# Kernel tuning notes

Hardware: AMD Instinct MI355X
Metric: run time of the kernel (lower is better)

Reference implementation:

```python
import jax, jax.numpy as jnp
import numpy as np

R = 8192            # reservoir_size
CORE = int(R * 0.6)          # 4915
SHELL = int(R * 0.3)         # 2457
FB = R - CORE - SHELL        # 820
H = 1024            # lstm_hidden
IN = 1              # input_size
OUT = 1             # output_size
LEAK = 0.1
SPECTRAL = 0.9
SPARSITY = 0.3


def _scaled(key, n):
    # uniform(-1,1) NxN; spectral radius of such a matrix ~ sqrt(n * var) = sqrt(n/3).
    # Scale to ~SPECTRAL (mimics the SVD-based scaling at init without the O(n^3) SVD).
    W = jax.random.uniform(key, (n, n), jnp.float32, -1.0, 1.0)
    return W * (SPECTRAL / jnp.sqrt(n / 3.0))


def setup_inputs() -> dict:
    key = jax.random.key(0)
    ks = jax.random.split(key, 20)
    u = lambda k, sh: jax.random.uniform(k, sh, jnp.float32, -1.0, 1.0)

    W_in = u(ks[0], (R, IN))
    W_core = _scaled(ks[1], CORE)
    mask_shell = (jax.random.uniform(ks[2], (SHELL, SHELL)) < SPARSITY).astype(jnp.float32)
    W_shell = _scaled(ks[3], SHELL) * mask_shell
    W_feedback = _scaled(ks[4], FB)
    W_shell_core = u(ks[5], (CORE, SHELL))
    W_feedback_core = u(ks[6], (CORE, FB))
    dopamine = jnp.float32(0.5)
    omega = jnp.ones((R,), jnp.float32) * 2.0
    gamma = jnp.ones((R,), jnp.float32) * 0.1

    # PyTorch LSTM params, gate order [i, f, g, o]
    s = 1.0 / np.sqrt(H)
    W_ih = jax.random.uniform(ks[7], (4 * H, R), jnp.float32, -s, s)
    W_hh = jax.random.uniform(ks[8], (4 * H, H), jnp.float32, -s, s)
    b_ih = jax.random.uniform(ks[9], (4 * H,), jnp.float32, -s, s)
    b_hh = jax.random.uniform(ks[10], (4 * H,), jnp.float32, -s, s)

    W_out = jax.random.uniform(ks[11], (OUT, H), jnp.float32, -s, s)
    b_out = jax.random.uniform(ks[12], (OUT,), jnp.float32, -s, s)

    x = jax.random.normal(ks[13], (IN,), jnp.float32)
    state = jax.random.normal(ks[14], (1, R), jnp.float32)
    lstm_hidden = jax.random.normal(ks[15], (1, 1, H), jnp.float32)
    lstm_cell = jax.random.normal(ks[16], (1, 1, H), jnp.float32)

    return dict(x=x, state=state, lstm_hidden=lstm_hidden, lstm_cell=lstm_cell,
                W_in=W_in, W_core=W_core, W_shell=W_shell, W_feedback=W_feedback,
                W_shell_core=W_shell_core, W_feedback_core=W_feedback_core,
                dopamine=dopamine, omega=omega, gamma=gamma,
                W_ih=W_ih, W_hh=W_hh, b_ih=b_ih, b_hh=b_hh,
                W_out=W_out, b_out=b_out)


def reference(x, state, lstm_hidden, lstm_cell,
              W_in, W_core, W_shell, W_feedback, W_shell_core, W_feedback_core,
              dopamine, omega, gamma, W_ih, W_hh, b_ih, b_hh, W_out, b_out):
    reservoir_in = W_in @ x                      # (R,)
    core = state[:, :CORE]                       # (1, CORE)
    shell = state[:, CORE:CORE + SHELL]          # (1, SHELL)
    fb = state[:, -FB:]                          # (1, FB)

    core_pred = jnp.tanh(core @ W_core.T + reservoir_in[:CORE][None, :])
    shell_pred = jnp.tanh(shell @ W_shell.T)
    fb_pred = jnp.tanh(fb @ W_feedback.T)
    core_pred = core_pred + jnp.tanh(shell_pred @ W_shell_core.T) \
                          + jnp.tanh(fb_pred @ W_feedback_core.T)

    core_new = (1.0 - LEAK) * core + LEAK * core_pred
    shell_new = (1.0 - LEAK) * shell + LEAK * shell_pred
    fb_new = (1.0 - LEAK) * fb + LEAK * fb_pred
    s = jnp.concatenate([core_new, shell_new, fb_new], axis=1)  # (1, R)

    # harmonic oscillator update + dopamine scaling
    s = s + 0.1 * (omega * s - gamma * jnp.tanh(s))
    s = dopamine * s

    # single LSTM cell step (torch gate order i, f, g, o)
    h = lstm_hidden[0]  # (1, H)
    c = lstm_cell[0]    # (1, H)
    gates = s @ W_ih.T + b_ih + h @ W_hh.T + b_hh   # (1, 4H)
    i, f, g, o = jnp.split(gates, 4, axis=1)
    c_new = jax.nn.sigmoid(f) * c + jax.nn.sigmoid(i) * jnp.tanh(g)
    h_new = jax.nn.sigmoid(o) * jnp.tanh(c_new)

    output = h_new @ W_out.T + b_out             # (1, OUT)
    return output, s, h_new[None], c_new[None]
```

## Files before the change

kernel.cpp:

```cpp
#include <hip/hip_runtime.h>
#include <math.h>

#define R_TOT 8192
#define CORE  4915
#define SHELL 2457
#define FB    820
#define H     1024

__device__ float g_pred1[R_TOT];
__device__ float g_s[R_TOT];
__device__ float g_gates[4 * H];

__device__ __forceinline__ int swz(int i) { return i + (i >> 5); }
#define SWZ_SIZE(n) ((n) + (((n) - 1) >> 5))

__device__ __forceinline__ float waveReduce(float v) {
  #pragma unroll
  for (int off = 32; off; off >>= 1) v += __shfl_down(v, off, 64);
  return v;
}

__device__ __forceinline__ float dotRow(const float* __restrict__ w,
                                        const float* __restrict__ xs,
                                        int xb, int N, int lane) {
  uintptr_t a = (uintptr_t)w;
  int head = (int)(((16 - (a & 15)) & 15) >> 2);
  if (head > N) head = N;
  float s0 = 0.f, s1 = 0.f, s2 = 0.f, s3 = 0.f;
  if (lane < head) s0 += w[lane] * xs[swz(xb + lane)];
  int nC = (N - head) >> 2;
  const float4* wv = (const float4*)(w + head);
  int b0 = xb + head;
  int c = lane;
  for (; c + 192 < nC; c += 256) {
    float4 v0 = wv[c], v1 = wv[c + 64], v2 = wv[c + 128], v3 = wv[c + 192];
    int i0 = b0 + (c << 2);
    s0 += v0.x*xs[swz(i0    )] + v0.y*xs[swz(i0+  1)] + v0.z*xs[swz(i0+  2)] + v0.w*xs[swz(i0+  3)];
    s1 += v1.x*xs[swz(i0+256)] + v1.y*xs[swz(i0+257)] + v1.z*xs[swz(i0+258)] + v1.w*xs[swz(i0+259)];
    s2 += v2.x*xs[swz(i0+512)] + v2.y*xs[swz(i0+513)] + v2.z*xs[swz(i0+514)] + v2.w*xs[swz(i0+515)];
    s3 += v3.x*xs[swz(i0+768)] + v3.y*xs[swz(i0+769)] + v3.z*xs[swz(i0+770)] + v3.w*xs[swz(i0+771)];
  }
  for (; c < nC; c += 64) {
    float4 v = wv[c];
    int i0 = b0 + (c << 2);
    s1 += v.x*xs[swz(i0)] + v.y*xs[swz(i0+1)] + v.z*xs[swz(i0+2)] + v.w*xs[swz(i0+3)];
  }
  for (int i = head + (nC << 2) + lane; i < N; i += 64)
    s2 += w[i] * xs[swz(xb + i)];
  return (s0 + s1) + (s2 + s3);
}

#define NB1_CORE  ((CORE  + 3) / 4)
#define NB1_SHELL ((SHELL + 3) / 4)
#define NB1_FB    ((FB    + 3) / 4)

__global__ __launch_bounds__(256, 8) void k_stage1(
    const float* __restrict__ state, const float* __restrict__ Wcore,
    const float* __restrict__ Wshell, const float* __restrict__ Wfb,
    const float* __restrict__ Win, const float* __restrict__ xin) {
  __shared__ float xs[SWZ_SIZE(CORE)];
  int b = blockIdx.x;
  int rowBase, N, xoff, isCore = 0;
  const float* W;
  if (b < NB1_CORE)                  { rowBase = b * 4;                         N = CORE;  xoff = 0;            W = Wcore; isCore = 1; }
  else if (b < NB1_CORE + NB1_SHELL) { rowBase = (b - NB1_CORE) * 4;            N = SHELL; xoff = CORE;         W = Wshell; }
  else                               { rowBase = (b - NB1_CORE - NB1_SHELL)*4;  N = FB;    xoff = CORE + SHELL; W = Wfb; }
  for (int i = threadIdx.x; i < N; i += 256) xs[swz(i)] = state[xoff + i];
  __syncthreads();
  int wave = threadIdx.x >> 6, lane = threadIdx.x & 63;
  int r = rowBase + wave;
  if (r >= N) return;
  float sum = waveReduce(dotRow(W + (size_t)r * N, xs, 0, N, lane));
  if (lane == 0) {
    if (isCore) sum += Win[r] * xin[0];
    g_pred1[xoff + r] = tanhf(sum);
  }
}

#define NB2_CORE ((CORE + 3) / 4)
#define NB2_EW   ((SHELL + FB + 255) / 256)

__device__ __forceinline__ void s_update(int i, float pred,
                                         const float* __restrict__ state,
                                         const float* __restrict__ omega,
                                         const float* __restrict__ gamma,
                                         float dopa, float* __restrict__ dout) {
  float old = state[i];
  float s1 = 0.9f * old + 0.1f * pred;
  float s2 = s1 + 0.1f * (omega[i] * s1 - gamma[i] * tanhf(s1));
  float s3 = dopa * s2;
  g_s[i] = s3;
  dout[1 + i] = s3;
}

__global__ __launch_bounds__(256, 8) void k_stage2(
    const float* __restrict__ state,
    const float* __restrict__ Wsc, const float* __restrict__ Wfc,
    const float* __restrict__ omega, const float* __restrict__ gamma,
    const float* __restrict__ dopamine, float* __restrict__ dout) {
  __shared__ float xs[SWZ_SIZE(SHELL + FB)];
  float dopa = dopamine[0];
  int b = blockIdx.x;
  if (b < NB2_CORE) {
    for (int i = threadIdx.x; i < SHELL + FB; i += 256) xs[swz(i)] = g_pred1[CORE + i];
    __syncthreads();
    int wave = threadIdx.x >> 6, lane = threadIdx.x & 63;
    int r = b * 4 + wave;
    if (r >= CORE) return;
    float d1 = waveReduce(dotRow(Wsc + (size_t)r * SHELL, xs, 0, SHELL, lane));
    float d2 = waveReduce(dotRow(Wfc + (size_t)r * FB, xs, SHELL, FB, lane));
    if (lane == 0) {
      float pred = g_pred1[r] + tanhf(d1) + tanhf(d2);
      s_update(r, pred, state, omega, gamma, dopa, dout);
    }
  } else {
    int i = CORE + (b - NB2_CORE) * 256 + threadIdx.x;
    if (i < R_TOT) s_update(i, g_pred1[i], state, omega, gamma, dopa, dout);
  }
}

__global__ __launch_bounds__(256, 4) void k_gates(
    const float* __restrict__ h,
    const float* __restrict__ Wih, const float* __restrict__ Whh,
    const float* __restrict__ bih, const float* __restrict__ bhh) {
  __shared__ float xs[SWZ_SIZE(R_TOT + H)];
  for (int i = threadIdx.x; i < R_TOT; i += 256) xs[swz(i)] = g_s[i];
  for (int i = threadIdx.x; i < H; i += 256) xs[swz(R_TOT + i)] = h[i];
  __syncthreads();
  int wave = threadIdx.x >> 6, lane = threadIdx.x & 63;
  int r = blockIdx.x * 4 + wave;
  float sum = dotRow(Wih + (size_t)r * R_TOT, xs, 0, R_TOT, lane)
            + dotRow(Whh + (size_t)r * H, xs, R_TOT, H, lane);
  sum = waveReduce(sum);
  if (lane == 0) g_gates[r] = sum + bih[r] + bhh[r];
}

__global__ __launch_bounds__(1024) void k_lstm(
    const float* __restrict__ c_in, const float* __restrict__ Wout,
    const float* __restrict__ bout, float* __restrict__ dout) {
  __shared__ float red[16];
  int j = threadIdx.x;
  float ig = g_gates[j], fg = g_gates[H + j], gg = g_gates[2 * H + j], og = g_gates[3 * H + j];
  float c = c_in[j];
  float cn = (1.f / (1.f + expf(-fg))) * c + (1.f / (1.f + expf(-ig))) * tanhf(gg);
  float hn = (1.f / (1.f + expf(-og))) * tanhf(cn);
  dout[1 + R_TOT + j] = hn;
  dout[1 + R_TOT + H + j] = cn;
  float w = Wout[j] * hn;
  w = waveReduce(w);
  int wave = j >> 6, lane = j & 63;
  if (lane == 0) red[wave] = w;
  __syncthreads();
  if (j == 0) {
    float t = 0.f;
    #pragma unroll
    for (int k = 0; k < 16; ++k) t += red[k];
    dout[0] = t + bout[0];
  }
}

extern "C" void kernel_launch(void* const* d_in, const int* in_sizes, int n_in,
                              void* d_out, int out_size, void* d_ws, size_t ws_size,
                              hipStream_t stream) {
  const float *x = 0, *state = 0, *h = 0, *c = 0, *Win = 0, *Wcore = 0, *Wshell = 0,
              *Wfb = 0, *Wsc = 0, *Wfc = 0, *dopa = 0, *omega = 0, *gamma = 0,
              *Wih = 0, *Whh = 0, *bih = 0, *bhh = 0, *Wout = 0, *bout = 0;
  int n1 = 0, n1024 = 0, n8192 = 0, n4096 = 0;
  for (int i = 0; i < n_in; ++i) {
    const float* p = (const float*)d_in[i];
    switch (in_sizes[i]) {
      case 24157225: Wcore = p; break;
      case 6036849:  Wshell = p; break;
      case 672400:   Wfb = p; break;
      case 12076155: Wsc = p; break;
      case 4030300:  Wfc = p; break;
      case 33554432: Wih = p; break;
      case 4194304:  Whh = p; break;
      case 1:    { if (n1 == 0) x = p; else if (n1 == 1) dopa = p; else bout = p; n1++; } break;
      case 1024: { if (n1024 == 0) h = p; else if (n1024 == 1) c = p; else Wout = p; n1024++; } break;
      case 8192: { if (n8192 == 0) state = p; else if (n8192 == 1) Win = p;
                   else if (n8192 == 2) omega = p; else gamma = p; n8192++; } break;
      case 4096: { if (n4096 == 0) bih = p; else bhh = p; n4096++; } break;
      default: break;
    }
  }
  float* dout = (float*)d_out;

  k_stage1<<<NB1_CORE + NB1_SHELL + NB1_FB, 256, 0, stream>>>(
      state, Wcore, Wshell, Wfb, Win, x);
  k_stage2<<<NB2_CORE + NB2_EW, 256, 0, stream>>>(
      state, Wsc, Wfc, omega, gamma, dopa, dout);
  k_gates<<<(4 * H) / 4, 256, 0, stream>>>(h, Wih, Whh, bih, bhh);
  k_lstm<<<1, 1024, 0, stream>>>(c, Wout, bout, dout);
}
```

Measured before the change: 367.4 us.

## Fuse all stages into one cooperative persistent kernel with atomic work queues

```diff
diff --git a/kernel.cpp b/kernel.cpp
--- a/kernel.cpp
+++ b/kernel.cpp
@@ -1,5 +1,8 @@
 #include <hip/hip_runtime.h>
+#include <hip/hip_cooperative_groups.h>
 #include <math.h>
+
+namespace cg = cooperative_groups;
 
 #define R_TOT 8192
 #define CORE  4915
@@ -7,9 +10,14 @@
 #define FB    820
 #define H     1024
 
-__device__ float g_pred1[R_TOT];
-__device__ float g_s[R_TOT];
-__device__ float g_gates[4 * H];
+#define NBLK  1024
+#define NTHR  256
+
+__device__ __align__(16) float g_pred1[R_TOT];
+__device__ __align__(16) float g_s[R_TOT];
+__device__ __align__(16) float g_gates[4 * H];
+__device__ int g_q1 = 0;
+__device__ int g_q2 = 0;
 
 __device__ __forceinline__ int swz(int i) { return i + (i >> 5); }
 #define SWZ_SIZE(n) ((n) + (((n) - 1) >> 5))
@@ -19,6 +27,8 @@
   for (int off = 32; off; off >>= 1) v += __shfl_down(v, off, 64);
   return v;
 }
+
+__device__ __forceinline__ float sigm(float x) { return 1.f / (1.f + expf(-x)); }
 
 __device__ __forceinline__ float dotRow(const float* __restrict__ w,
                                         const float* __restrict__ xs,
@@ -50,6 +60,146 @@
   return (s0 + s1) + (s2 + s3);
 }
 
+__device__ __forceinline__ void s_update(int i, float pred,
+                                         const float* __restrict__ state,
+                                         const float* __restrict__ omega,
+                                         const float* __restrict__ gamma,
+                                         float dopa, float* __restrict__ dout) {
+  float old = state[i];
+  float s1 = 0.9f * old + 0.1f * pred;
+  float s2 = s1 + 0.1f * (omega[i] * s1 - gamma[i] * tanhf(s1));
+  float s3 = dopa * s2;
+  g_s[i] = s3;
+  dout[1 + i] = s3;
+}
+
+#define P1_SHELL0 CORE
+#define P1_WHH0   (CORE + SHELL)
+#define P1_FB0    (CORE + SHELL + 4 * H)
+#define P1_N      (CORE + SHELL + 4 * H + FB)
+
+__global__ __launch_bounds__(NTHR, 4) void k_fused(
+    const float* __restrict__ state, const float* __restrict__ Wcore,
+    const float* __restrict__ Wshell, const float* __restrict__ Wfb,
+    const float* __restrict__ Win, const float* __restrict__ xin,
+    const float* __restrict__ Wsc, const float* __restrict__ Wfc,
+    const float* __restrict__ omega, const float* __restrict__ gamma,
+    const float* __restrict__ dopamine,
+    const float* __restrict__ Wih, const float* __restrict__ Whh,
+    const float* __restrict__ bih, const float* __restrict__ bhh,
+    const float* __restrict__ hin, const float* __restrict__ cin,
+    const float* __restrict__ Wout, const float* __restrict__ bout,
+    float* __restrict__ dout) {
+  __shared__ float xs[SWZ_SIZE(R_TOT + H)];
+  __shared__ float red[4];
+  cg::grid_group grid = cg::this_grid();
+  const int tid = threadIdx.x, wave = tid >> 6, lane = tid & 63;
+
+  {
+    const float4* s4 = (const float4*)state;
+    for (int i = tid; i < R_TOT / 4; i += NTHR) {
+      float4 v = s4[i]; int b = i << 2;
+      xs[swz(b)] = v.x; xs[swz(b+1)] = v.y; xs[swz(b+2)] = v.z; xs[swz(b+3)] = v.w;
+    }
+    const float4* h4 = (const float4*)hin;
+    for (int i = tid; i < H / 4; i += NTHR) {
+      float4 v = h4[i]; int b = R_TOT + (i << 2);
+      xs[swz(b)] = v.x; xs[swz(b+1)] = v.y; xs[swz(b+2)] = v.z; xs[swz(b+3)] = v.w;
+    }
+  }
+  __syncthreads();
+  const float x0 = xin[0];
+
+  for (;;) {
+    int idx;
+    if (lane == 0) idx = atomicAdd(&g_q1, 1);
+    idx = __shfl(idx, 0, 64);
+    if (idx >= P1_N) break;
+    const float* w; int xb, N; float* dst; float pre = 0.f; int doT = 1;
+    if (idx < P1_SHELL0) {
+      w = Wcore + (size_t)idx * CORE; xb = 0; N = CORE;
+      dst = g_pred1 + idx; pre = Win[idx] * x0;
+    } else if (idx < P1_WHH0) {
+      int r = idx - P1_SHELL0;
+      w = Wshell + (size_t)r * SHELL; xb = CORE; N = SHELL;
+      dst = g_pred1 + CORE + r;
+    } else if (idx < P1_FB0) {
+      int r = idx - P1_WHH0;
+      w = Whh + (size_t)r * H; xb = R_TOT; N = H;
+      dst = g_gates + r; doT = 0;
+    } else {
+      int r = idx - P1_FB0;
+      w = Wfb + (size_t)r * FB; xb = CORE + SHELL; N = FB;
+      dst = g_pred1 + CORE + SHELL + r;
+    }
+    float sum = waveReduce(dotRow(w, xs, xb, N, lane)) + pre;
+    if (lane == 0) *dst = doT ? tanhf(sum) : sum;
+  }
+
+  grid.sync();
+
+  if (blockIdx.x == 0 && tid == 0) atomicExch(&g_q1, 0);
+  const float dopa = dopamine[0];
+  {
+    int gt = blockIdx.x * NTHR + tid;
+    if (gt < SHELL + FB) {
+      int i = CORE + gt;
+      s_update(i, g_pred1[i], state, omega, gamma, dopa, dout);
+    }
+  }
+  for (int i = tid; i < SHELL + FB; i += NTHR) xs[swz(i)] = g_pred1[CORE + i];
+  __syncthreads();
+  for (;;) {
+    int idx;
+    if (lane == 0) idx = atomicAdd(&g_q2, 1);
+    idx = __shfl(idx, 0, 64);
+    if (idx >= CORE) break;
+    float d1 = waveReduce(dotRow(Wsc + (size_t)idx * SHELL, xs, 0, SHELL, lane));
+    float d2 = waveReduce(dotRow(Wfc + (size_t)idx * FB, xs, SHELL, FB, lane));
+    if (lane == 0) {
+      float pred = g_pred1[idx] + tanhf(d1) + tanhf(d2);
+      s_update(idx, pred, state, omega, gamma, dopa, dout);
+    }
+  }
+
+  grid.sync();
+
+  if (blockIdx.x == 0 && tid == 0) atomicExch(&g_q2, 0);
+  {
+    const float4* s4 = (const float4*)g_s;
+    for (int i = tid; i < R_TOT / 4; i += NTHR) {
+      float4 v = s4[i]; int b = i << 2;
+      xs[swz(b)] = v.x; xs[swz(b+1)] = v.y; xs[swz(b+2)] = v.z; xs[swz(b+3)] = v.w;
+    }
+  }
+  __syncthreads();
+  {
+    int r = blockIdx.x * 4 + wave;
+    float sum = waveReduce(dotRow(Wih + (size_t)r * R_TOT, xs, 0, R_TOT, lane));
+    if (lane == 0) g_gates[r] += sum + bih[r] + bhh[r];
+  }
+
+  grid.sync();
+
+  if (blockIdx.x == 0) {
+    float acc = 0.f;
+    for (int j = tid; j < H; j += NTHR) {
+      float ig = g_gates[j], fg = g_gates[H + j];
+      float gg = g_gates[2 * H + j], og = g_gates[3 * H + j];
+      float c = cin[j];
+      float cn = sigm(fg) * c + sigm(ig) * tanhf(gg);
+      float hn = sigm(og) * tanhf(cn);
+      dout[1 + R_TOT + j] = hn;
+      dout[1 + R_TOT + H + j] = cn;
+      acc += Wout[j] * hn;
+    }
+    acc = waveReduce(acc);
+    if (lane == 0) red[wave] = acc;
+    __syncthreads();
+    if (tid == 0) dout[0] = red[0] + red[1] + red[2] + red[3] + bout[0];
+  }
+}
+
 #define NB1_CORE  ((CORE  + 3) / 4)
 #define NB1_SHELL ((SHELL + 3) / 4)
 #define NB1_FB    ((FB    + 3) / 4)
@@ -79,19 +229,6 @@
 
 #define NB2_CORE ((CORE + 3) / 4)
 #define NB2_EW   ((SHELL + FB + 255) / 256)
-
-__device__ __forceinline__ void s_update(int i, float pred,
-                                         const float* __restrict__ state,
-                                         const float* __restrict__ omega,
-                                         const float* __restrict__ gamma,
-                                         float dopa, float* __restrict__ dout) {
-  float old = state[i];
-  float s1 = 0.9f * old + 0.1f * pred;
-  float s2 = s1 + 0.1f * (omega[i] * s1 - gamma[i] * tanhf(s1));
-  float s3 = dopa * s2;
-  g_s[i] = s3;
-  dout[1 + i] = s3;
-}
 
 __global__ __launch_bounds__(256, 8) void k_stage2(
     const float* __restrict__ state,
@@ -138,23 +275,23 @@
 __global__ __launch_bounds__(1024) void k_lstm(
     const float* __restrict__ c_in, const float* __restrict__ Wout,
     const float* __restrict__ bout, float* __restrict__ dout) {
-  __shared__ float red[16];
+  __shared__ float red16[16];
   int j = threadIdx.x;
   float ig = g_gates[j], fg = g_gates[H + j], gg = g_gates[2 * H + j], og = g_gates[3 * H + j];
   float c = c_in[j];
-  float cn = (1.f / (1.f + expf(-fg))) * c + (1.f / (1.f + expf(-ig))) * tanhf(gg);
-  float hn = (1.f / (1.f + expf(-og))) * tanhf(cn);
+  float cn = sigm(fg) * c + sigm(ig) * tanhf(gg);
+  float hn = sigm(og) * tanhf(cn);
   dout[1 + R_TOT + j] = hn;
   dout[1 + R_TOT + H + j] = cn;
   float w = Wout[j] * hn;
   w = waveReduce(w);
   int wave = j >> 6, lane = j & 63;
-  if (lane == 0) red[wave] = w;
+  if (lane == 0) red16[wave] = w;
   __syncthreads();
   if (j == 0) {
     float t = 0.f;
     #pragma unroll
-    for (int k = 0; k < 16; ++k) t += red[k];
+    for (int k = 0; k < 16; ++k) t += red16[k];
     dout[0] = t + bout[0];
   }
 }
@@ -186,10 +323,20 @@
   }
   float* dout = (float*)d_out;
 
-  k_stage1<<<NB1_CORE + NB1_SHELL + NB1_FB, 256, 0, stream>>>(
-      state, Wcore, Wshell, Wfb, Win, x);
-  k_stage2<<<NB2_CORE + NB2_EW, 256, 0, stream>>>(
-      state, Wsc, Wfc, omega, gamma, dopa, dout);
-  k_gates<<<(4 * H) / 4, 256, 0, stream>>>(h, Wih, Whh, bih, bhh);
-  k_lstm<<<1, 1024, 0, stream>>>(c, Wout, bout, dout);
-}
+  void* args[] = {(void*)&state, (void*)&Wcore, (void*)&Wshell, (void*)&Wfb,
+                  (void*)&Win, (void*)&x, (void*)&Wsc, (void*)&Wfc,
+                  (void*)&omega, (void*)&gamma, (void*)&dopa,
+                  (void*)&Wih, (void*)&Whh, (void*)&bih, (void*)&bhh,
+                  (void*)&h, (void*)&c, (void*)&Wout, (void*)&bout, (void*)&dout};
+  hipError_t e = hipLaunchCooperativeKernel((void*)k_fused, dim3(NBLK), dim3(NTHR),
+                                            args, 0, stream);
+  if (e != hipSuccess) {
+    (void)hipGetLastError();
+    k_stage1<<<NB1_CORE + NB1_SHELL + NB1_FB, 256, 0, stream>>>(
+        state, Wcore, Wshell, Wfb, Win, x);
+    k_stage2<<<NB2_CORE + NB2_EW, 256, 0, stream>>>(
+        state, Wsc, Wfc, omega, gamma, dopa, dout);
+    k_gates<<<(4 * H) / 4, 256, 0, stream>>>(h, Wih, Whh, bih, bhh);
+    k_lstm<<<1, 1024, 0, stream>>>(c, Wout, bout, dout);
+  }
+}
```

Result: slower. 968.0 us (+163.5%).

## Move W_hh matvec into stage 1 and use aligned float4 dot paths

Applied to the files above, without the earlier changes.

```diff
diff --git a/kernel.cpp b/kernel.cpp
--- a/kernel.cpp
+++ b/kernel.cpp
@@ -7,9 +7,9 @@
 #define FB    820
 #define H     1024
 
-__device__ float g_pred1[R_TOT];
-__device__ float g_s[R_TOT];
-__device__ float g_gates[4 * H];
+__device__ __align__(16) float g_pred1[R_TOT];
+__device__ __align__(16) float g_s[R_TOT];
+__device__ __align__(16) float g_gates[4 * H];
 
 __device__ __forceinline__ int swz(int i) { return i + (i >> 5); }
 #define SWZ_SIZE(n) ((n) + (((n) - 1) >> 5))
@@ -20,18 +20,37 @@
   return v;
 }
 
-__device__ __forceinline__ float dotRow(const float* __restrict__ w,
-                                        const float* __restrict__ xs,
-                                        int xb, int N, int lane) {
+__device__ __forceinline__ float sigm(float x) { return 1.f / (1.f + expf(-x)); }
+__device__ __forceinline__ float dot4(float4 a, float4 b) {
+  return a.x * b.x + a.y * b.y + a.z * b.z + a.w * b.w;
+}
+
+__device__ __forceinline__ float dotRowSw(const float* __restrict__ w,
+                                          const float* __restrict__ xs,
+                                          int xb, int N, int lane) {
   uintptr_t a = (uintptr_t)w;
   int head = (int)(((16 - (a & 15)) & 15) >> 2);
   if (head > N) head = N;
-  float s0 = 0.f, s1 = 0.f, s2 = 0.f, s3 = 0.f;
+  float s0 = 0.f, s1 = 0.f, s2 = 0.f, s3 = 0.f,
+        s4 = 0.f, s5 = 0.f, s6 = 0.f, s7 = 0.f;
   if (lane < head) s0 += w[lane] * xs[swz(xb + lane)];
   int nC = (N - head) >> 2;
   const float4* wv = (const float4*)(w + head);
   int b0 = xb + head;
   int c = lane;
+  for (; c + 448 < nC; c += 512) {
+    float4 v0 = wv[c],       v1 = wv[c + 64],  v2 = wv[c + 128], v3 = wv[c + 192],
+           v4 = wv[c + 256], v5 = wv[c + 320], v6 = wv[c + 384], v7 = wv[c + 448];
+    int i0 = b0 + (c << 2);
+    s0 += v0.x*xs[swz(i0     )] + v0.y*xs[swz(i0+   1)] + v0.z*xs[swz(i0+   2)] + v0.w*xs[swz(i0+   3)];
+    s1 += v1.x*xs[swz(i0+ 256)] + v1.y*xs[swz(i0+ 257)] + v1.z*xs[swz(i0+ 258)] + v1.w*xs[swz(i0+ 259)];
+    s2 += v2.x*xs[swz(i0+ 512)] + v2.y*xs[swz(i0+ 513)] + v2.z*xs[swz(i0+ 514)] + v2.w*xs[swz(i0+ 515)];
+    s3 += v3.x*xs[swz(i0+ 768)] + v3.y*xs[swz(i0+ 769)] + v3.z*xs[swz(i0+ 770)] + v3.w*xs[swz(i0+ 771)];
+    s4 += v4.x*xs[swz(i0+1024)] + v4.y*xs[swz(i0+1025)] + v4.z*xs[swz(i0+1026)] + v4.w*xs[swz(i0+1027)];
+    s5 += v5.x*xs[swz(i0+1280)] + v5.y*xs[swz(i0+1281)] + v5.z*xs[swz(i0+1282)] + v5.w*xs[swz(i0+1283)];
+    s6 += v6.x*xs[swz(i0+1536)] + v6.y*xs[swz(i0+1537)] + v6.z*xs[swz(i0+1538)] + v6.w*xs[swz(i0+1539)];
+    s7 += v7.x*xs[swz(i0+1792)] + v7.y*xs[swz(i0+1793)] + v7.z*xs[swz(i0+1794)] + v7.w*xs[swz(i0+1795)];
+  }
   for (; c + 192 < nC; c += 256) {
     float4 v0 = wv[c], v1 = wv[c + 64], v2 = wv[c + 128], v3 = wv[c + 192];
     int i0 = b0 + (c << 2);
@@ -47,38 +66,31 @@
   }
   for (int i = head + (nC << 2) + lane; i < N; i += 64)
     s2 += w[i] * xs[swz(xb + i)];
-  return (s0 + s1) + (s2 + s3);
-}
-
-#define NB1_CORE  ((CORE  + 3) / 4)
-#define NB1_SHELL ((SHELL + 3) / 4)
-#define NB1_FB    ((FB    + 3) / 4)
-
-__global__ __launch_bounds__(256, 8) void k_stage1(
-    const float* __restrict__ state, const float* __restrict__ Wcore,
-    const float* __restrict__ Wshell, const float* __restrict__ Wfb,
-    const float* __restrict__ Win, const float* __restrict__ xin) {
-  __shared__ float xs[SWZ_SIZE(CORE)];
-  int b = blockIdx.x;
-  int rowBase, N, xoff, isCore = 0;
-  const float* W;
-  if (b < NB1_CORE)                  { rowBase = b * 4;                         N = CORE;  xoff = 0;            W = Wcore; isCore = 1; }
-  else if (b < NB1_CORE + NB1_SHELL) { rowBase = (b - NB1_CORE) * 4;            N = SHELL; xoff = CORE;         W = Wshell; }
-  else                               { rowBase = (b - NB1_CORE - NB1_SHELL)*4;  N = FB;    xoff = CORE + SHELL; W = Wfb; }
-  for (int i = threadIdx.x; i < N; i += 256) xs[swz(i)] = state[xoff + i];
-  __syncthreads();
-  int wave = threadIdx.x >> 6, lane = threadIdx.x & 63;
-  int r = rowBase + wave;
-  if (r >= N) return;
-  float sum = waveReduce(dotRow(W + (size_t)r * N, xs, 0, N, lane));
-  if (lane == 0) {
-    if (isCore) sum += Win[r] * xin[0];
-    g_pred1[xoff + r] = tanhf(sum);
-  }
-}
-
-#define NB2_CORE ((CORE + 3) / 4)
-#define NB2_EW   ((SHELL + FB + 255) / 256)
+  return ((s0 + s1) + (s2 + s3)) + ((s4 + s5) + (s6 + s7));
+}
+
+__device__ __forceinline__ float dotRowAl(const float4* __restrict__ wv,
+                                          const float4* __restrict__ xs4,
+                                          int nC, int lane) {
+  float s0 = 0.f, s1 = 0.f, s2 = 0.f, s3 = 0.f,
+        s4 = 0.f, s5 = 0.f, s6 = 0.f, s7 = 0.f;
+  int c = lane;
+  for (; c + 448 < nC; c += 512) {
+    float4 v0 = wv[c],       v1 = wv[c + 64],  v2 = wv[c + 128], v3 = wv[c + 192],
+           v4 = wv[c + 256], v5 = wv[c + 320], v6 = wv[c + 384], v7 = wv[c + 448];
+    s0 += dot4(v0, xs4[c      ]); s1 += dot4(v1, xs4[c + 64 ]);
+    s2 += dot4(v2, xs4[c + 128]); s3 += dot4(v3, xs4[c + 192]);
+    s4 += dot4(v4, xs4[c + 256]); s5 += dot4(v5, xs4[c + 320]);
+    s6 += dot4(v6, xs4[c + 384]); s7 += dot4(v7, xs4[c + 448]);
+  }
+  for (; c + 192 < nC; c += 256) {
+    float4 v0 = wv[c], v1 = wv[c + 64], v2 = wv[c + 128], v3 = wv[c + 192];
+    s0 += dot4(v0, xs4[c      ]); s1 += dot4(v1, xs4[c + 64 ]);
+    s2 += dot4(v2, xs4[c + 128]); s3 += dot4(v3, xs4[c + 192]);
+  }
+  for (; c < nC; c += 64) s1 += dot4(wv[c], xs4[c]);
+  return ((s0 + s1) + (s2 + s3)) + ((s4 + s5) + (s6 + s7));
+}
 
 __device__ __forceinline__ void s_update(int i, float pred,
                                          const float* __restrict__ state,
@@ -93,46 +105,98 @@
   dout[1 + i] = s3;
 }
 
-__global__ __launch_bounds__(256, 8) void k_stage2(
+#define NB1_CORE  ((CORE  + 3) / 4)
+#define NB1_SHELL ((SHELL + 3) / 4)
+#define NB1_WHH   (4 * H / 4)
+#define NB1_FB    ((FB    + 3) / 4)
+#define NB1_TOT   (NB1_CORE + NB1_SHELL + NB1_WHH + NB1_FB)
+
+__global__ __launch_bounds__(256, 4) void k_stage1(
+    const float* __restrict__ state, const float* __restrict__ Wcore,
+    const float* __restrict__ Wshell, const float* __restrict__ Wfb,
+    const float* __restrict__ Win, const float* __restrict__ xin,
+    const float* __restrict__ Whh, const float* __restrict__ hin) {
+  __shared__ __align__(16) float xs[SWZ_SIZE(CORE)];
+  int b = blockIdx.x;
+  int tid = threadIdx.x, wave = tid >> 6, lane = tid & 63;
+  if (b < NB1_CORE) {
+    for (int i = tid; i < CORE; i += 256) xs[swz(i)] = state[i];
+    __syncthreads();
+    int r = b * 4 + wave;
+    if (r >= CORE) return;
+    float sum = waveReduce(dotRowSw(Wcore + (size_t)r * CORE, xs, 0, CORE, lane));
+    if (lane == 0) g_pred1[r] = tanhf(sum + Win[r] * xin[0]);
+  } else if (b < NB1_CORE + NB1_SHELL) {
+    for (int i = tid; i < SHELL; i += 256) xs[swz(i)] = state[CORE + i];
+    __syncthreads();
+    int r = (b - NB1_CORE) * 4 + wave;
+    if (r >= SHELL) return;
+    float sum = waveReduce(dotRowSw(Wshell + (size_t)r * SHELL, xs, 0, SHELL, lane));
+    if (lane == 0) g_pred1[CORE + r] = tanhf(sum);
+  } else if (b < NB1_CORE + NB1_SHELL + NB1_WHH) {
+    float4* xs4 = (float4*)xs;
+    const float4* h4 = (const float4*)hin;
+    for (int i = tid; i < H / 4; i += 256) xs4[i] = h4[i];
+    __syncthreads();
+    int r = (b - NB1_CORE - NB1_SHELL) * 4 + wave;
+    float sum = waveReduce(dotRowAl((const float4*)(Whh + (size_t)r * H), xs4, H / 4, lane));
+    if (lane == 0) g_gates[r] = sum;
+  } else {
+    float4* xs4 = (float4*)xs;
+    const float4* f4 = (const float4*)(state + CORE + SHELL);
+    for (int i = tid; i < FB / 4; i += 256) xs4[i] = f4[i];
+    __syncthreads();
+    int r = (b - NB1_CORE - NB1_SHELL - NB1_WHH) * 4 + wave;
+    if (r >= FB) return;
+    float sum = waveReduce(dotRowAl((const float4*)(Wfb + (size_t)r * FB), xs4, FB / 4, lane));
+    if (lane == 0) g_pred1[CORE + SHELL + r] = tanhf(sum);
+  }
+}
+
+#define NB2_CORE ((CORE + 3) / 4)
+#define NB2_EW   ((SHELL + FB + 255) / 256)
+
+__global__ __launch_bounds__(256, 4) void k_stage2(
     const float* __restrict__ state,
     const float* __restrict__ Wsc, const float* __restrict__ Wfc,
     const float* __restrict__ omega, const float* __restrict__ gamma,
     const float* __restrict__ dopamine, float* __restrict__ dout) {
-  __shared__ float xs[SWZ_SIZE(SHELL + FB)];
+  __shared__ __align__(16) float  xsS[SWZ_SIZE(SHELL)];
+  __shared__ __align__(16) float4 xsF[FB / 4];
   float dopa = dopamine[0];
-  int b = blockIdx.x;
+  int b = blockIdx.x, tid = threadIdx.x;
   if (b < NB2_CORE) {
-    for (int i = threadIdx.x; i < SHELL + FB; i += 256) xs[swz(i)] = g_pred1[CORE + i];
-    __syncthreads();
-    int wave = threadIdx.x >> 6, lane = threadIdx.x & 63;
+    for (int i = tid; i < SHELL; i += 256) xsS[swz(i)] = g_pred1[CORE + i];
+    const float4* f4 = (const float4*)(g_pred1 + CORE + SHELL);
+    for (int i = tid; i < FB / 4; i += 256) xsF[i] = f4[i];
+    __syncthreads();
+    int wave = tid >> 6, lane = tid & 63;
     int r = b * 4 + wave;
     if (r >= CORE) return;
-    float d1 = waveReduce(dotRow(Wsc + (size_t)r * SHELL, xs, 0, SHELL, lane));
-    float d2 = waveReduce(dotRow(Wfc + (size_t)r * FB, xs, SHELL, FB, lane));
+    float d1 = waveReduce(dotRowSw(Wsc + (size_t)r * SHELL, xsS, 0, SHELL, lane));
+    float d2 = waveReduce(dotRowAl((const float4*)(Wfc + (size_t)r * FB), xsF, FB / 4, lane));
     if (lane == 0) {
       float pred = g_pred1[r] + tanhf(d1) + tanhf(d2);
       s_update(r, pred, state, omega, gamma, dopa, dout);
     }
   } else {
-    int i = CORE + (b - NB2_CORE) * 256 + threadIdx.x;
+    int i = CORE + (b - NB2_CORE) * 256 + tid;
     if (i < R_TOT) s_update(i, g_pred1[i], state, omega, gamma, dopa, dout);
   }
 }
 
 __global__ __launch_bounds__(256, 4) void k_gates(
-    const float* __restrict__ h,
-    const float* __restrict__ Wih, const float* __restrict__ Whh,
+    const float* __restrict__ Wih,
     const float* __restrict__ bih, const float* __restrict__ bhh) {
-  __shared__ float xs[SWZ_SIZE(R_TOT + H)];
-  for (int i = threadIdx.x; i < R_TOT; i += 256) xs[swz(i)] = g_s[i];
-  for (int i = threadIdx.x; i < H; i += 256) xs[swz(R_TOT + i)] = h[i];
+  __shared__ __align__(16) float4 xs4[R_TOT / 4];
+  int tid = threadIdx.x;
+  const float4* s4 = (const float4*)g_s;
+  for (int i = tid; i < R_TOT / 4; i += 256) xs4[i] = s4[i];
   __syncthreads();
-  int wave = threadIdx.x >> 6, lane = threadIdx.x & 63;
+  int wave = tid >> 6, lane = tid & 63;
   int r = blockIdx.x * 4 + wave;
-  float sum = dotRow(Wih + (size_t)r * R_TOT, xs, 0, R_TOT, lane)
-            + dotRow(Whh + (size_t)r * H, xs, R_TOT, H, lane);
-  sum = waveReduce(sum);
-  if (lane == 0) g_gates[r] = sum + bih[r] + bhh[r];
+  float sum = waveReduce(dotRowAl((const float4*)(Wih + (size_t)r * R_TOT), xs4, R_TOT / 4, lane));
+  if (lane == 0) g_gates[r] += sum + bih[r] + bhh[r];
 }
 
 __global__ __launch_bounds__(1024) void k_lstm(
@@ -142,8 +206,8 @@
   int j = threadIdx.x;
   float ig = g_gates[j], fg = g_gates[H + j], gg = g_gates[2 * H + j], og = g_gates[3 * H + j];
   float c = c_in[j];
-  float cn = (1.f / (1.f + expf(-fg))) * c + (1.f / (1.f + expf(-ig))) * tanhf(gg);
-  float hn = (1.f / (1.f + expf(-og))) * tanhf(cn);
+  float cn = sigm(fg) * c + sigm(ig) * tanhf(gg);
+  float hn = sigm(og) * tanhf(cn);
   dout[1 + R_TOT + j] = hn;
   dout[1 + R_TOT + H + j] = cn;
   float w = Wout[j] * hn;
@@ -186,10 +250,8 @@
   }
   float* dout = (float*)d_out;
 
-  k_stage1<<<NB1_CORE + NB1_SHELL + NB1_FB, 256, 0, stream>>>(
-      state, Wcore, Wshell, Wfb, Win, x);
-  k_stage2<<<NB2_CORE + NB2_EW, 256, 0, stream>>>(
-      state, Wsc, Wfc, omega, gamma, dopa, dout);
-  k_gates<<<(4 * H) / 4, 256, 0, stream>>>(h, Wih, Whh, bih, bhh);
+  k_stage1<<<NB1_TOT, 256, 0, stream>>>(state, Wcore, Wshell, Wfb, Win, x, Whh, h);
+  k_stage2<<<NB2_CORE + NB2_EW, 256, 0, stream>>>(state, Wsc, Wfc, omega, gamma, dopa, dout);
+  k_gates<<<(4 * H) / 4, 256, 0, stream>>>(Wih, bih, bhh);
   k_lstm<<<1, 1024, 0, stream>>>(c, Wout, bout, dout);
 }
```

Measured after the change: 367.0 us. About the same (-0.1%).
